# Kernel tuning notes

Measured on AMD Instinct MI355X. Metric: run time of the kernel, lower is better.

The kernel has to match this reference:

```python
import jax, jax.numpy as jnp
import numpy as np

N_NODES = 100000
N_EDGES = 1600000
D_IN = 64
D_OUT = 64


def setup_inputs() -> dict:
    key = jax.random.key(0)
    k1, k2, k3, k4, k5 = jax.random.split(key, 5)
    feat = jax.random.normal(k1, (N_NODES, D_IN), dtype=jnp.float32)
    src = jax.random.randint(k2, (N_EDGES,), 0, N_NODES, dtype=jnp.int32)
    dst = jax.random.randint(k3, (N_EDGES,), 0, N_NODES, dtype=jnp.int32)
    W = jax.random.normal(k4, (D_OUT, D_IN), dtype=jnp.float32) * (1.0 / np.sqrt(D_IN))
    b = jax.random.normal(k5, (D_OUT,), dtype=jnp.float32) * 0.01
    return {"feat": feat, "src": src, "dst": dst, "W": W, "b": b}


def reference(feat, src, dst, W, b):
    n = feat.shape[0]
    ones = jnp.ones(src.shape[0], dtype=feat.dtype)
    # out-degree normalization on source features (deg^{-1/2}, clamp min 1)
    deg_out = jnp.clip(jax.ops.segment_sum(ones, src, num_segments=n), 1.0)
    h = feat * jax.lax.rsqrt(deg_out)[:, None]  # [N, D_in]
    # copy_src + sum aggregation over edges (gather from src, scatter-add to dst)
    agg = jax.ops.segment_sum(h[src], dst, num_segments=n)  # [N, D_in]
    # dense linear
    rst = agg @ W.T + b  # [N, D_out]
    # in-degree normalization on destination
    deg_in = jnp.clip(jax.ops.segment_sum(ones, dst, num_segments=n), 1.0)
    return rst * jax.lax.rsqrt(deg_in)[:, None]
```

## Files before the change

kernel.cpp:

```cpp
#include <hip/hip_runtime.h>
#include <hip/hip_bf16.h>

#define N_NODES 100000
#define N_EDGES 1600000
#define D 64

#define NB 160
#define CH (N_EDGES / NB)
#define BSH 6
#define BNODES 64
#define NBUCK 1563
#define NBUCKP 1568
#define BCAP 2560

#define GK_BLOCKS 4096

#define NPART 8
#define PART_N (N_NODES / NPART)
#define TOTAL_I4 (N_EDGES / 4)
#define SCAN_BS 256
#define SCAN_ITEMS 4
#define SCAN_TILE (SCAN_BS * SCAN_ITEMS)
#define SCAN_NBLK ((N_NODES + SCAN_TILE - 1) / SCAN_TILE)

typedef unsigned short ushort8v __attribute__((ext_vector_type(8)));

__device__ __forceinline__ unsigned short f2bf_rne(float f) {
    unsigned u = __float_as_uint(f);
    u += 0x7fffu + ((u >> 16) & 1u);
    return (unsigned short)(u >> 16);
}

__global__ void __launch_bounds__(512) hist_kernel(const int* __restrict__ src,
                                                   const int* __restrict__ dst,
                                                   unsigned int* __restrict__ Hs,
                                                   unsigned int* __restrict__ Hd) {
    __shared__ unsigned hs[NBUCKP], hd[NBUCKP];
    int t = threadIdx.x;
    for (int i = t; i < NBUCKP; i += 512) { hs[i] = 0u; hd[i] = 0u; }
    __syncthreads();
    int base = blockIdx.x * CH;
    for (int i = base + t; i < base + CH; i += 512) {
        atomicAdd(&hs[(unsigned)src[i] >> BSH], 1u);
        atomicAdd(&hd[(unsigned)dst[i] >> BSH], 1u);
    }
    __syncthreads();
    unsigned int* rs = Hs + (size_t)blockIdx.x * NBUCKP;
    unsigned int* rd = Hd + (size_t)blockIdx.x * NBUCKP;
    for (int i = t; i < NBUCKP; i += 512) { rs[i] = hs[i]; rd[i] = hd[i]; }
}

__global__ void __launch_bounds__(256) colscan_kernel(unsigned int* __restrict__ H,
                                                      unsigned int* __restrict__ total) {
    __shared__ unsigned sh[256];
    int b = blockIdx.x;
    int t = threadIdx.x;
    unsigned v = (t < NB) ? H[(size_t)t * NBUCKP + b] : 0u;
    sh[t] = v;
    __syncthreads();
    for (int off = 1; off < 256; off <<= 1) {
        unsigned x = (t >= off) ? sh[t - off] : 0u;
        __syncthreads();
        sh[t] += x;
        __syncthreads();
    }
    if (t < NB) H[(size_t)t * NBUCKP + b] = sh[t] - v;
    if (t == NB - 1) total[b] = sh[t];
}

__global__ void __launch_bounds__(1024) totscan_kernel(const unsigned int* __restrict__ total_s,
                                                       unsigned int* __restrict__ cbase_s,
                                                       const unsigned int* __restrict__ total_d,
                                                       unsigned int* __restrict__ cbase_d) {
    __shared__ unsigned sh[1024];
    __shared__ unsigned carry;
    int t = threadIdx.x;
    for (int arr = 0; arr < 2; ++arr) {
        const unsigned int* tot = arr ? total_d : total_s;
        unsigned int* cb = arr ? cbase_d : cbase_s;
        if (t == 0) carry = 0u;
        __syncthreads();
        for (int chunk = 0; chunk < NBUCKP; chunk += 1024) {
            int i = chunk + t;
            unsigned v = (i < NBUCKP) ? tot[i] : 0u;
            sh[t] = v;
            __syncthreads();
            for (int off = 1; off < 1024; off <<= 1) {
                unsigned x = (t >= off) ? sh[t - off] : 0u;
                __syncthreads();
                sh[t] += x;
                __syncthreads();
            }
            unsigned c0 = carry;
            if (i < NBUCKP) cb[i] = c0 + sh[t] - v;
            __syncthreads();
            if (t == 1023) carry = c0 + sh[1023];
            __syncthreads();
        }
    }
}

__global__ void __launch_bounds__(512) scatter_kernel(const int* __restrict__ src,
                                                      const int* __restrict__ dst,
                                                      const unsigned int* __restrict__ Hs,
                                                      const unsigned int* __restrict__ Hd,
                                                      const unsigned int* __restrict__ cbase_s,
                                                      const unsigned int* __restrict__ cbase_d,
                                                      unsigned int* __restrict__ sbuck,
                                                      unsigned int* __restrict__ dbuck) {
    __shared__ unsigned cs[NBUCKP], cd[NBUCKP];
    int t = threadIdx.x;
    int blk = blockIdx.x;
    const unsigned int* rs = Hs + (size_t)blk * NBUCKP;
    const unsigned int* rd = Hd + (size_t)blk * NBUCKP;
    for (int i = t; i < NBUCKP; i += 512) {
        cs[i] = cbase_s[i] + rs[i];
        cd[i] = cbase_d[i] + rd[i];
    }
    __syncthreads();
    int base = blk * CH;
    for (int i = base + t; i < base + CH; i += 512) {
        unsigned s = (unsigned)src[i];
        unsigned d = (unsigned)dst[i];
        unsigned ps = atomicAdd(&cs[s >> BSH], 1u);
        sbuck[ps] = s & (BNODES - 1);
        unsigned pd = atomicAdd(&cd[d >> BSH], 1u);
        dbuck[pd] = ((d & (BNODES - 1)) << 17) | s;
    }
}

__global__ void __launch_bounds__(256) degcnt_kernel(const unsigned int* __restrict__ sbuck,
                                                     const unsigned int* __restrict__ cbase_s,
                                                     const unsigned int* __restrict__ total_s,
                                                     unsigned int* __restrict__ deg_out) {
    __shared__ unsigned cnt[BNODES];
    int bk = blockIdx.x;
    int t = threadIdx.x;
    if (t < BNODES) cnt[t] = 0u;
    __syncthreads();
    unsigned base = cbase_s[bk];
    unsigned n = total_s[bk];
    for (unsigned i = t; i < n; i += 256) {
        atomicAdd(&cnt[sbuck[base + i]], 1u);
    }
    __syncthreads();
    int node = bk * BNODES + t;
    if (t < BNODES && node < N_NODES) deg_out[node] = cnt[t];
}

__global__ void __launch_bounds__(256) g_kernel(const float* __restrict__ feat,
                                                const unsigned int* __restrict__ deg_out,
                                                const float* __restrict__ W,
                                                unsigned short* __restrict__ g) {
    int t = threadIdx.x;
    int w = t >> 6;
    int lane = t & 63;

    float wreg[D];
    #pragma unroll
    for (int q = 0; q < 16; ++q) {
        const float4 t4 = *reinterpret_cast<const float4*>(&W[(size_t)lane * D + q * 4]);
        wreg[q * 4 + 0] = t4.x;
        wreg[q * 4 + 1] = t4.y;
        wreg[q * 4 + 2] = t4.z;
        wreg[q * 4 + 3] = t4.w;
    }

    for (int r = blockIdx.x * 4 + w; r < N_NODES; r += GK_BLOCKS * 4) {
        unsigned int dg = deg_out[r];
        float sc = rsqrtf((float)(dg > 0u ? dg : 1u));
        float fv = feat[(size_t)r * D + lane] * sc;
        float o = 0.f;
        #pragma unroll
        for (int k = 0; k < D; ++k) {
            float fk = __int_as_float(
                __builtin_amdgcn_readlane(__float_as_int(fv), k));
            o += fk * wreg[k];
        }
        g[(size_t)r * D + lane] = f2bf_rne(o);
    }
}

__global__ void __launch_bounds__(256) gsum_bucket(const unsigned short* __restrict__ g,
                                                   const unsigned int* __restrict__ dbuck,
                                                   const unsigned int* __restrict__ cbase_d,
                                                   const unsigned int* __restrict__ total_d,
                                                   const float* __restrict__ b,
                                                   float* __restrict__ out) {
    __shared__ int binned[BCAP];
    __shared__ unsigned cnt[BNODES], offs[BNODES], cur[BNODES];
    int bk = blockIdx.x;
    int t = threadIdx.x;
    int w = t >> 6;
    int lane = t & 63;
    int slot = lane >> 3;
    int sub  = lane & 7;

    if (t < BNODES) cnt[t] = 0u;
    __syncthreads();

    unsigned base = cbase_d[bk];
    unsigned n = total_d[bk];
    if (n > (unsigned)BCAP) n = BCAP;

    for (unsigned i = t; i < n; i += 256) {
        atomicAdd(&cnt[dbuck[base + i] >> 17], 1u);
    }
    __syncthreads();
    if (t < BNODES) offs[t] = cnt[t];
    __syncthreads();
    for (int off = 1; off < BNODES; off <<= 1) {
        unsigned x = (t >= off && t < BNODES) ? offs[t - off] : 0u;
        __syncthreads();
        if (t < BNODES) offs[t] += x;
        __syncthreads();
    }
    if (t < BNODES) cur[t] = offs[t] - cnt[t];
    __syncthreads();
    for (unsigned i = t; i < n; i += 256) {
        unsigned p = dbuck[base + i];
        unsigned d = p >> 17;
        unsigned pos = atomicAdd(&cur[d], 1u);
        binned[pos] = (int)(p & 0x1FFFFu);
    }
    __syncthreads();

    float breg = b[sub * 8 + slot];
    for (int nl = w; nl < BNODES; nl += 4) {
        int node = bk * BNODES + nl;
        if (node >= N_NODES) break;
        unsigned deg = cnt[nl];
        unsigned eoff = offs[nl] - deg;

        float acc[8];
        #pragma unroll
        for (int j = 0; j < 8; ++j) acc[j] = 0.f;

        for (unsigned b64 = 0; b64 < deg; b64 += 64u) {
            int c = (int)(deg - b64);
            if (c > 64) c = 64;
            int myidx = (lane < c) ? binned[eoff + b64 + lane] : 0;
            for (int e = 0; e < c; e += 8) {
                int es = e + slot;
                int s = __shfl(myidx, es);
                if (es < c) {
                    const ushort8v v = *reinterpret_cast<const ushort8v*>(
                        &g[(size_t)s * D + sub * 8]);
                    #pragma unroll
                    for (int j = 0; j < 8; ++j) {
                        acc[j] += __uint_as_float((unsigned)v[j] << 16);
                    }
                }
            }
        }

        #pragma unroll
        for (int j = 0; j < 8; ++j) {
            acc[j] += __shfl_xor(acc[j], 8);
            acc[j] += __shfl_xor(acc[j], 16);
            acc[j] += __shfl_xor(acc[j], 32);
        }
        float red = (slot == 0) ? acc[0] : (slot == 1) ? acc[1] :
                    (slot == 2) ? acc[2] : (slot == 3) ? acc[3] :
                    (slot == 4) ? acc[4] : (slot == 5) ? acc[5] :
                    (slot == 6) ? acc[6] : acc[7];
        int X = sub * 8 + slot;
        float rs = rsqrtf((float)(deg > 0u ? deg : 1u));
        __builtin_nontemporal_store((red + breg) * rs,
                                    out + (size_t)node * D + X);
    }
}

__global__ void __launch_bounds__(256) deg2_part(const int* __restrict__ src,
                                                 const int* __restrict__ dst,
                                                 unsigned int* __restrict__ deg_out,
                                                 unsigned int* __restrict__ deg_in) {
    int part  = blockIdx.x & (NPART - 1);
    int chunk = blockIdx.x >> 3;
    unsigned lo = (unsigned)(part * PART_N);
    int base = chunk * (TOTAL_I4 / 250);
    for (int i = base + (int)threadIdx.x; i < base + (TOTAL_I4 / 250); i += 256) {
        const int4 s4 = reinterpret_cast<const int4*>(src)[i];
        const int4 d4 = reinterpret_cast<const int4*>(dst)[i];
        if ((unsigned)(s4.x - lo) < (unsigned)PART_N) atomicAdd(&deg_out[s4.x], 1u);
        if ((unsigned)(s4.y - lo) < (unsigned)PART_N) atomicAdd(&deg_out[s4.y], 1u);
        if ((unsigned)(s4.z - lo) < (unsigned)PART_N) atomicAdd(&deg_out[s4.z], 1u);
        if ((unsigned)(s4.w - lo) < (unsigned)PART_N) atomicAdd(&deg_out[s4.w], 1u);
        if ((unsigned)(d4.x - lo) < (unsigned)PART_N) atomicAdd(&deg_in[d4.x], 1u);
        if ((unsigned)(d4.y - lo) < (unsigned)PART_N) atomicAdd(&deg_in[d4.y], 1u);
        if ((unsigned)(d4.z - lo) < (unsigned)PART_N) atomicAdd(&deg_in[d4.z], 1u);
        if ((unsigned)(d4.w - lo) < (unsigned)PART_N) atomicAdd(&deg_in[d4.w], 1u);
    }
}

__global__ void __launch_bounds__(SCAN_BS) scan1_kernel(
        const unsigned int* __restrict__ in,
        unsigned int* __restrict__ out,
        unsigned int* __restrict__ partials, int n) {
    __shared__ unsigned int ssum[SCAN_BS];
    int t = threadIdx.x;
    int base = blockIdx.x * SCAN_TILE + t * SCAN_ITEMS;
    unsigned int v[SCAN_ITEMS];
    unsigned int s = 0;
    #pragma unroll
    for (int k = 0; k < SCAN_ITEMS; ++k) {
        v[k] = (base + k < n) ? in[base + k] : 0u;
        s += v[k];
    }
    ssum[t] = s;
    __syncthreads();
    for (int off = 1; off < SCAN_BS; off <<= 1) {
        unsigned int x = (t >= off) ? ssum[t - off] : 0u;
        __syncthreads();
        ssum[t] += x;
        __syncthreads();
    }
    unsigned int excl = (t == 0) ? 0u : ssum[t - 1];
    if (t == SCAN_BS - 1) partials[blockIdx.x] = ssum[t];
    unsigned int run = excl;
    #pragma unroll
    for (int k = 0; k < SCAN_ITEMS; ++k) {
        if (base + k < n) out[base + k] = run;
        run += v[k];
    }
}

__global__ void __launch_bounds__(128) scan2_kernel(
        unsigned int* __restrict__ partials, int nb) {
    __shared__ unsigned int sh[128];
    int t = threadIdx.x;
    unsigned int v = (t < nb) ? partials[t] : 0u;
    sh[t] = v;
    __syncthreads();
    for (int off = 1; off < 128; off <<= 1) {
        unsigned int x = (t >= off) ? sh[t - off] : 0u;
        __syncthreads();
        sh[t] += x;
        __syncthreads();
    }
    if (t < nb) partials[t] = (t == 0) ? 0u : sh[t - 1];
}

__global__ void scan3_kernel(unsigned int* __restrict__ offsets,
                             const unsigned int* __restrict__ partials,
                             unsigned int* __restrict__ cursor, int n) {
    int i = blockIdx.x * blockDim.x + threadIdx.x;
    if (i < n) {
        unsigned int v = offsets[i] + partials[i / SCAN_TILE];
        offsets[i] = v;
        cursor[i]  = v;
    }
    if (i == 0) offsets[n] = N_EDGES;
}

__global__ void __launch_bounds__(256) place_part(const int* __restrict__ src,
                                                  const int* __restrict__ dst,
                                                  unsigned int* __restrict__ cursor,
                                                  int* __restrict__ sorted_src) {
    int part  = blockIdx.x & (NPART - 1);
    int chunk = blockIdx.x >> 3;
    unsigned lo = (unsigned)(part * PART_N);
    int base = chunk * (TOTAL_I4 / 250);
    for (int i = base + (int)threadIdx.x; i < base + (TOTAL_I4 / 250); i += 256) {
        const int4 s4 = reinterpret_cast<const int4*>(src)[i];
        const int4 d4 = reinterpret_cast<const int4*>(dst)[i];
        #define PLACE1(S, Dd)                                             \
            if ((unsigned)((unsigned)(Dd) - lo) < (unsigned)PART_N) {     \
                unsigned p = atomicAdd(&cursor[(Dd)], 1u);                \
                sorted_src[p] = (S);                                      \
            }
        PLACE1(s4.x, d4.x)
        PLACE1(s4.y, d4.y)
        PLACE1(s4.z, d4.z)
        PLACE1(s4.w, d4.w)
        #undef PLACE1
    }
}

__global__ void h_kernel(const float* __restrict__ feat,
                         const unsigned int* __restrict__ deg_out,
                         unsigned short* __restrict__ h) {
    int tid = blockIdx.x * blockDim.x + threadIdx.x;
    if (tid >= N_NODES * 16) return;
    int node = tid >> 4;
    unsigned int dg = deg_out[node];
    float sc = rsqrtf((float)(dg > 0u ? dg : 1u));
    const float4 v = *reinterpret_cast<const float4*>(&feat[(size_t)tid * 4]);
    ushort4 o;
    o.x = f2bf_rne(v.x * sc);
    o.y = f2bf_rne(v.y * sc);
    o.z = f2bf_rne(v.z * sc);
    o.w = f2bf_rne(v.w * sc);
    *reinterpret_cast<ushort4*>(&h[(size_t)tid * 4]) = o;
}

__global__ void __launch_bounds__(256) gg2_kernel(
        const unsigned short* __restrict__ h,
        const int* __restrict__ sorted_src,
        const unsigned int* __restrict__ offsets,
        const float* __restrict__ W,
        const float* __restrict__ b,
        float* __restrict__ out) {
    int t = threadIdx.x;
    int w = t >> 6;
    int lane = t & 63;
    int slot = lane >> 3;
    int sub  = lane & 7;

    float wreg[D];
    #pragma unroll
    for (int q = 0; q < 16; ++q) {
        const float4 t4 = *reinterpret_cast<const float4*>(&W[(size_t)lane * D + q * 4]);
        wreg[q * 4 + 0] = t4.x;
        wreg[q * 4 + 1] = t4.y;
        wreg[q * 4 + 2] = t4.z;
        wreg[q * 4 + 3] = t4.w;
    }
    float breg = b[lane];

    for (int r = blockIdx.x * 4 + w; r < N_NODES; r += GK_BLOCKS * 4) {
        unsigned int beg = offsets[r];
        unsigned int end = offsets[r + 1];
        unsigned int deg = end - beg;

        float acc[8];
        #pragma unroll
        for (int j = 0; j < 8; ++j) acc[j] = 0.f;

        for (unsigned int base = beg; base < end; base += 64u) {
            int count = (int)(end - base);
            if (count > 64) count = 64;
            int myidx = (lane < count) ? sorted_src[base + lane] : 0;
            for (int e = 0; e < count; e += 8) {
                int es = e + slot;
                int s = __shfl(myidx, es);
                if (es < count) {
                    const ushort8v v = *reinterpret_cast<const ushort8v*>(
                        &h[(size_t)s * D + sub * 8]);
                    #pragma unroll
                    for (int j = 0; j < 8; ++j) {
                        acc[j] += __uint_as_float((unsigned)v[j] << 16);
                    }
                }
            }
        }

        #pragma unroll
        for (int j = 0; j < 8; ++j) {
            acc[j] += __shfl_xor(acc[j], 8);
            acc[j] += __shfl_xor(acc[j], 16);
            acc[j] += __shfl_xor(acc[j], 32);
        }

        float o = breg;
        #pragma unroll
        for (int k = 0; k < D; ++k) {
            float av = __int_as_float(
                __builtin_amdgcn_readlane(__float_as_int(acc[k & 7]), k >> 3));
            o += av * wreg[k];
        }

        out[(size_t)r * D + lane] = o * rsqrtf((float)(deg > 0u ? deg : 1u));
    }
}

extern "C" void kernel_launch(void* const* d_in, const int* in_sizes, int n_in,
                              void* d_out, int out_size, void* d_ws, size_t ws_size,
                              hipStream_t stream) {
    const float* feat = (const float*)d_in[0];
    const int*   src  = (const int*)d_in[1];
    const int*   dst  = (const int*)d_in[2];
    const float* W    = (const float*)d_in[3];
    const float* b    = (const float*)d_in[4];
    float* out = (float*)d_out;

    {
        unsigned int* Hs      = (unsigned int*)d_ws;
        unsigned int* Hd      = Hs + (size_t)NB * NBUCKP;
        unsigned int* total_s = Hd + (size_t)NB * NBUCKP;
        unsigned int* cbase_s = total_s + NBUCKP;
        unsigned int* total_d = cbase_s + NBUCKP;
        unsigned int* cbase_d = total_d + NBUCKP;
        unsigned int* deg_out = cbase_d + NBUCKP;
        unsigned int* sbuck   = deg_out + N_NODES;
        unsigned int* dbuck   = sbuck + N_EDGES;
        unsigned short* g     = (unsigned short*)(dbuck + N_EDGES);
        size_t need_A = ((size_t)2 * NB * NBUCKP + 4 * NBUCKP + N_NODES +
                         (size_t)2 * N_EDGES + (size_t)N_NODES * D / 2) * 4;
        if (ws_size >= need_A) {
            hist_kernel<<<NB, 512, 0, stream>>>(src, dst, Hs, Hd);
            colscan_kernel<<<NBUCKP, 256, 0, stream>>>(Hs, total_s);
            colscan_kernel<<<NBUCKP, 256, 0, stream>>>(Hd, total_d);
            totscan_kernel<<<1, 1024, 0, stream>>>(total_s, cbase_s, total_d, cbase_d);
            scatter_kernel<<<NB, 512, 0, stream>>>(src, dst, Hs, Hd,
                                                   cbase_s, cbase_d, sbuck, dbuck);
            degcnt_kernel<<<NBUCK, 256, 0, stream>>>(sbuck, cbase_s, total_s, deg_out);
            g_kernel<<<GK_BLOCKS, 256, 0, stream>>>(feat, deg_out, W, g);
            gsum_bucket<<<NBUCK, 256, 0, stream>>>(g, dbuck, cbase_d, total_d, b, out);
            return;
        }
    }

    unsigned int* deg_out  = (unsigned int*)d_ws;
    unsigned int* deg_in   = deg_out + N_NODES;
    unsigned int* offsets  = deg_in + N_NODES;
    unsigned int* cursor   = offsets + N_NODES + 1;
    unsigned int* partials = cursor + N_NODES;
    size_t hdr = (size_t)(4 * N_NODES + 1 + 128);
    hdr = (hdr + 3u) & ~(size_t)3;
    int* sorted_src = (int*)d_ws + hdr;
    size_t hoff = hdr + N_EDGES;
    unsigned short* h = (unsigned short*)((unsigned int*)d_ws + hoff);

    hipMemsetAsync(d_ws, 0, (size_t)2 * N_NODES * sizeof(unsigned int), stream);
    deg2_part<<<2000, 256, 0, stream>>>(src, dst, deg_out, deg_in);
    scan1_kernel<<<SCAN_NBLK, SCAN_BS, 0, stream>>>(deg_in, offsets, partials, N_NODES);
    scan2_kernel<<<1, 128, 0, stream>>>(partials, SCAN_NBLK);
    scan3_kernel<<<(N_NODES + 255) / 256, 256, 0, stream>>>(offsets, partials, cursor, N_NODES);
    h_kernel<<<(N_NODES * 16 + 255) / 256, 256, 0, stream>>>(feat, deg_out, h);
    place_part<<<2000, 256, 0, stream>>>(src, dst, cursor, sorted_src);
    gg2_kernel<<<GK_BLOCKS, 256, 0, stream>>>(h, sorted_src, offsets, W, b, out);
}
```

Measured before the change: 164.8 us.

## Fuse scans and degree counting into fewer kernels, use atomic bucket bases

Merges the two column-scan launches into one, and replaces the single-block total scan with an atomic cursor that hands out bucket base offsets, so buckets are no longer in sorted order. Degree counting is fused into the feature-transform kernel, which removes the deg_out buffer and one launch. The aggregation kernel moves to 512 threads, keeps the bucket entries in shared memory instead of re-reading them, and reads neighbour indices straight from shared memory rather than through shuffles. This cuts launch count and serial scan latency, but bucket placement now depends on atomic ordering and the work is spread across fewer blocks.

```diff
diff --git a/kernel.cpp b/kernel.cpp
--- a/kernel.cpp
+++ b/kernel.cpp
@@ -13,11 +13,10 @@
 #define NBUCKP 1568
 #define BCAP 2560
 
-#define GK_BLOCKS 4096
-
 #define NPART 8
 #define PART_N (N_NODES / NPART)
 #define TOTAL_I4 (N_EDGES / 4)
+#define GK_BLOCKS 4096
 #define SCAN_BS 256
 #define SCAN_ITEMS 4
 #define SCAN_TILE (SCAN_BS * SCAN_ITEMS)
@@ -34,9 +33,11 @@
 __global__ void __launch_bounds__(512) hist_kernel(const int* __restrict__ src,
                                                    const int* __restrict__ dst,
                                                    unsigned int* __restrict__ Hs,
-                                                   unsigned int* __restrict__ Hd) {
+                                                   unsigned int* __restrict__ Hd,
+                                                   unsigned int* __restrict__ cursors) {
     __shared__ unsigned hs[NBUCKP], hd[NBUCKP];
     int t = threadIdx.x;
+    if (blockIdx.x == 0 && t < 8) cursors[t] = 0u;
     for (int i = t; i < NBUCKP; i += 512) { hs[i] = 0u; hd[i] = 0u; }
     __syncthreads();
     int base = blockIdx.x * CH;
@@ -50,10 +51,19 @@
     for (int i = t; i < NBUCKP; i += 512) { rs[i] = hs[i]; rd[i] = hd[i]; }
 }
 
-__global__ void __launch_bounds__(256) colscan_kernel(unsigned int* __restrict__ H,
-                                                      unsigned int* __restrict__ total) {
+__global__ void __launch_bounds__(256) colscan2_kernel(unsigned int* __restrict__ Hs,
+                                                       unsigned int* __restrict__ Hd,
+                                                       unsigned int* __restrict__ total_s,
+                                                       unsigned int* __restrict__ total_d,
+                                                       unsigned int* __restrict__ cbase_s,
+                                                       unsigned int* __restrict__ cbase_d,
+                                                       unsigned int* __restrict__ cursors) {
     __shared__ unsigned sh[256];
-    int b = blockIdx.x;
+    int arr = (blockIdx.x >= NBUCKP) ? 1 : 0;
+    int b = blockIdx.x - arr * NBUCKP;
+    unsigned int* H      = arr ? Hd : Hs;
+    unsigned int* total  = arr ? total_d : total_s;
+    unsigned int* cbase  = arr ? cbase_d : cbase_s;
     int t = threadIdx.x;
     unsigned v = (t < NB) ? H[(size_t)t * NBUCKP + b] : 0u;
     sh[t] = v;
@@ -65,38 +75,9 @@
         __syncthreads();
     }
     if (t < NB) H[(size_t)t * NBUCKP + b] = sh[t] - v;
-    if (t == NB - 1) total[b] = sh[t];
-}
-
-__global__ void __launch_bounds__(1024) totscan_kernel(const unsigned int* __restrict__ total_s,
-                                                       unsigned int* __restrict__ cbase_s,
-                                                       const unsigned int* __restrict__ total_d,
-                                                       unsigned int* __restrict__ cbase_d) {
-    __shared__ unsigned sh[1024];
-    __shared__ unsigned carry;
-    int t = threadIdx.x;
-    for (int arr = 0; arr < 2; ++arr) {
-        const unsigned int* tot = arr ? total_d : total_s;
-        unsigned int* cb = arr ? cbase_d : cbase_s;
-        if (t == 0) carry = 0u;
-        __syncthreads();
-        for (int chunk = 0; chunk < NBUCKP; chunk += 1024) {
-            int i = chunk + t;
-            unsigned v = (i < NBUCKP) ? tot[i] : 0u;
-            sh[t] = v;
-            __syncthreads();
-            for (int off = 1; off < 1024; off <<= 1) {
-                unsigned x = (t >= off) ? sh[t - off] : 0u;
-                __syncthreads();
-                sh[t] += x;
-                __syncthreads();
-            }
-            unsigned c0 = carry;
-            if (i < NBUCKP) cb[i] = c0 + sh[t] - v;
-            __syncthreads();
-            if (t == 1023) carry = c0 + sh[1023];
-            __syncthreads();
-        }
+    if (t == NB - 1) {
+        total[b] = sh[t];
+        cbase[b] = atomicAdd(&cursors[arr], sh[t]);
     }
 }
 
@@ -129,32 +110,24 @@
     }
 }
 
-__global__ void __launch_bounds__(256) degcnt_kernel(const unsigned int* __restrict__ sbuck,
-                                                     const unsigned int* __restrict__ cbase_s,
-                                                     const unsigned int* __restrict__ total_s,
-                                                     unsigned int* __restrict__ deg_out) {
+__global__ void __launch_bounds__(512) gprep_kernel(const unsigned int* __restrict__ sbuck,
+                                                    const unsigned int* __restrict__ cbase_s,
+                                                    const unsigned int* __restrict__ total_s,
+                                                    const float* __restrict__ feat,
+                                                    const float* __restrict__ W,
+                                                    unsigned short* __restrict__ g) {
     __shared__ unsigned cnt[BNODES];
     int bk = blockIdx.x;
     int t = threadIdx.x;
+    int w = t >> 6;
+    int lane = t & 63;
     if (t < BNODES) cnt[t] = 0u;
     __syncthreads();
     unsigned base = cbase_s[bk];
     unsigned n = total_s[bk];
-    for (unsigned i = t; i < n; i += 256) {
+    for (unsigned i = t; i < n; i += 512) {
         atomicAdd(&cnt[sbuck[base + i]], 1u);
     }
-    __syncthreads();
-    int node = bk * BNODES + t;
-    if (t < BNODES && node < N_NODES) deg_out[node] = cnt[t];
-}
-
-__global__ void __launch_bounds__(256) g_kernel(const float* __restrict__ feat,
-                                                const unsigned int* __restrict__ deg_out,
-                                                const float* __restrict__ W,
-                                                unsigned short* __restrict__ g) {
-    int t = threadIdx.x;
-    int w = t >> 6;
-    int lane = t & 63;
 
     float wreg[D];
     #pragma unroll
@@ -165,11 +138,14 @@
         wreg[q * 4 + 2] = t4.z;
         wreg[q * 4 + 3] = t4.w;
     }
-
-    for (int r = blockIdx.x * 4 + w; r < N_NODES; r += GK_BLOCKS * 4) {
-        unsigned int dg = deg_out[r];
+    __syncthreads();
+
+    for (int nl = w; nl < BNODES; nl += 8) {
+        int node = bk * BNODES + nl;
+        if (node >= N_NODES) break;
+        unsigned dg = cnt[nl];
         float sc = rsqrtf((float)(dg > 0u ? dg : 1u));
-        float fv = feat[(size_t)r * D + lane] * sc;
+        float fv = feat[(size_t)node * D + lane] * sc;
         float o = 0.f;
         #pragma unroll
         for (int k = 0; k < D; ++k) {
@@ -177,16 +153,17 @@
                 __builtin_amdgcn_readlane(__float_as_int(fv), k));
             o += fk * wreg[k];
         }
-        g[(size_t)r * D + lane] = f2bf_rne(o);
-    }
-}
-
-__global__ void __launch_bounds__(256) gsum_bucket(const unsigned short* __restrict__ g,
+        g[(size_t)node * D + lane] = f2bf_rne(o);
+    }
+}
+
+__global__ void __launch_bounds__(512) gsum_bucket(const unsigned short* __restrict__ g,
                                                    const unsigned int* __restrict__ dbuck,
                                                    const unsigned int* __restrict__ cbase_d,
                                                    const unsigned int* __restrict__ total_d,
                                                    const float* __restrict__ b,
                                                    float* __restrict__ out) {
+    __shared__ unsigned raw[BCAP];
     __shared__ int binned[BCAP];
     __shared__ unsigned cnt[BNODES], offs[BNODES], cur[BNODES];
     int bk = blockIdx.x;
@@ -203,30 +180,31 @@
     unsigned n = total_d[bk];
     if (n > (unsigned)BCAP) n = BCAP;
 
-    for (unsigned i = t; i < n; i += 256) {
-        atomicAdd(&cnt[dbuck[base + i] >> 17], 1u);
+    for (unsigned i = t; i < n; i += 512) {
+        unsigned p = dbuck[base + i];
+        raw[i] = p;
+        atomicAdd(&cnt[p >> 17], 1u);
     }
     __syncthreads();
     if (t < BNODES) offs[t] = cnt[t];
     __syncthreads();
     for (int off = 1; off < BNODES; off <<= 1) {
-        unsigned x = (t >= off && t < BNODES) ? offs[t - off] : 0u;
+        unsigned x = (t < BNODES && t >= off) ? offs[t - off] : 0u;
         __syncthreads();
         if (t < BNODES) offs[t] += x;
         __syncthreads();
     }
     if (t < BNODES) cur[t] = offs[t] - cnt[t];
     __syncthreads();
-    for (unsigned i = t; i < n; i += 256) {
-        unsigned p = dbuck[base + i];
-        unsigned d = p >> 17;
-        unsigned pos = atomicAdd(&cur[d], 1u);
+    for (unsigned i = t; i < n; i += 512) {
+        unsigned p = raw[i];
+        unsigned pos = atomicAdd(&cur[p >> 17], 1u);
         binned[pos] = (int)(p & 0x1FFFFu);
     }
     __syncthreads();
 
     float breg = b[sub * 8 + slot];
-    for (int nl = w; nl < BNODES; nl += 4) {
+    for (int nl = w; nl < BNODES; nl += 8) {
         int node = bk * BNODES + nl;
         if (node >= N_NODES) break;
         unsigned deg = cnt[nl];
@@ -236,20 +214,15 @@
         #pragma unroll
         for (int j = 0; j < 8; ++j) acc[j] = 0.f;
 
-        for (unsigned b64 = 0; b64 < deg; b64 += 64u) {
-            int c = (int)(deg - b64);
-            if (c > 64) c = 64;
-            int myidx = (lane < c) ? binned[eoff + b64 + lane] : 0;
-            for (int e = 0; e < c; e += 8) {
-                int es = e + slot;
-                int s = __shfl(myidx, es);
-                if (es < c) {
-                    const ushort8v v = *reinterpret_cast<const ushort8v*>(
-                        &g[(size_t)s * D + sub * 8]);
-                    #pragma unroll
-                    for (int j = 0; j < 8; ++j) {
-                        acc[j] += __uint_as_float((unsigned)v[j] << 16);
-                    }
+        for (unsigned e = 0; e < deg; e += 8u) {
+            unsigned es = e + (unsigned)slot;
+            if (es < deg) {
+                int s = binned[eoff + es];
+                const ushort8v v = *reinterpret_cast<const ushort8v*>(
+                    &g[(size_t)s * D + sub * 8]);
+                #pragma unroll
+                for (int j = 0; j < 8; ++j) {
+                    acc[j] += __uint_as_float((unsigned)v[j] << 16);
                 }
             }
         }
@@ -481,22 +454,20 @@
         unsigned int* cbase_s = total_s + NBUCKP;
         unsigned int* total_d = cbase_s + NBUCKP;
         unsigned int* cbase_d = total_d + NBUCKP;
-        unsigned int* deg_out = cbase_d + NBUCKP;
-        unsigned int* sbuck   = deg_out + N_NODES;
+        unsigned int* cursors = cbase_d + NBUCKP;
+        unsigned int* sbuck   = cursors + 8;
         unsigned int* dbuck   = sbuck + N_EDGES;
         unsigned short* g     = (unsigned short*)(dbuck + N_EDGES);
-        size_t need_A = ((size_t)2 * NB * NBUCKP + 4 * NBUCKP + N_NODES +
+        size_t need_A = ((size_t)2 * NB * NBUCKP + 4 * NBUCKP + 8 +
                          (size_t)2 * N_EDGES + (size_t)N_NODES * D / 2) * 4;
         if (ws_size >= need_A) {
-            hist_kernel<<<NB, 512, 0, stream>>>(src, dst, Hs, Hd);
-            colscan_kernel<<<NBUCKP, 256, 0, stream>>>(Hs, total_s);
-            colscan_kernel<<<NBUCKP, 256, 0, stream>>>(Hd, total_d);
-            totscan_kernel<<<1, 1024, 0, stream>>>(total_s, cbase_s, total_d, cbase_d);
+            hist_kernel<<<NB, 512, 0, stream>>>(src, dst, Hs, Hd, cursors);
+            colscan2_kernel<<<2 * NBUCKP, 256, 0, stream>>>(Hs, Hd, total_s, total_d,
+                                                            cbase_s, cbase_d, cursors);
             scatter_kernel<<<NB, 512, 0, stream>>>(src, dst, Hs, Hd,
                                                    cbase_s, cbase_d, sbuck, dbuck);
-            degcnt_kernel<<<NBUCK, 256, 0, stream>>>(sbuck, cbase_s, total_s, deg_out);
-            g_kernel<<<GK_BLOCKS, 256, 0, stream>>>(feat, deg_out, W, g);
-            gsum_bucket<<<NBUCK, 256, 0, stream>>>(g, dbuck, cbase_d, total_d, b, out);
+            gprep_kernel<<<NBUCK, 512, 0, stream>>>(sbuck, cbase_s, total_s, feat, W, g);
+            gsum_bucket<<<NBUCK, 512, 0, stream>>>(g, dbuck, cbase_d, total_d, b, out);
             return;
         }
     }
```

Result: slower. 190.6 us (+15.7%).
